# Kernel optimization log

Measured on AMD Instinct MI355X. Metric: run time of the kernel, lower is better.

The kernel has to match this reference:

```python
import jax, jax.numpy as jnp
import numpy as np

N_FFT = 2048
HOP = 512
WIN = 2048
PAD = N_FFT // 2  # center padding, n_fft // 2


def setup_inputs() -> dict:
    key = jax.random.key(0)
    x = jax.random.normal(key, (16, 262144), dtype=jnp.float32)
    # periodic Hann window, identical to torch.hann_window(2048)
    window = (0.5 - 0.5 * jnp.cos(2.0 * jnp.pi * jnp.arange(WIN) / WIN)).astype(jnp.float32)
    return {"x": x, "window": window}


def reference(x, window):
    # x: [B, T]; center reflect-pad by n_fft//2 on both sides (matches F.pad mode='reflect')
    xp = jnp.pad(x, ((0, 0), (PAD, PAD)), mode="reflect")
    n_frames = (xp.shape[-1] - N_FFT) // HOP + 1  # static
    # strided framing (replaces the identity-conv im2col in the original)
    idx = jnp.arange(n_frames)[:, None] * HOP + jnp.arange(N_FFT)[None, :]  # [F, n_fft]
    frames = xp[:, idx] * window  # [B, F, n_fft], windowed frames
    # windowed DFT; rfft of windowed frame == F.linear(frames, fft_k) in the original
    spec = jnp.fft.rfft(frames, axis=-1)  # [B, F, n_fft//2+1] complex
    real = jnp.real(spec).transpose(0, 2, 1)  # [B, dim, F]
    imag = jnp.imag(spec).transpose(0, 2, 1)  # [B, dim, F]
    return (real, imag)
```

## Files before the change

### kernel.cpp

```cpp
#include <hip/hip_runtime.h>


#define N_FFT   2048
#define LOG2N   11
#define HOP     512
#define PADL    1024
#define NBINS   1025
#define NFRAMES 513
#define NBATCH  16
#define TLEN    262144

#define HALF_OUT ((size_t)NBATCH * NBINS * NFRAMES)

__device__ __forceinline__ int pidx(int a) { return a + (a >> 5); }

__device__ __forceinline__ int refl(int j) {
    if (j < 0)          j = -j;
    else if (j >= TLEN) j = 2 * TLEN - 2 - j;
    return j;
}

__device__ __forceinline__ float2 cmul(float2 a, float2 w) {
    return make_float2(fmaf(a.x, w.x, -a.y * w.y), fmaf(a.x, w.y, a.y * w.x));
}
__device__ __forceinline__ float2 cadd(float2 a, float2 b) {
    return make_float2(a.x + b.x, a.y + b.y);
}
__device__ __forceinline__ float2 csub(float2 a, float2 b) {
    return make_float2(a.x - b.x, a.y - b.y);
}
__device__ __forceinline__ float2 csqr(float2 w) {
    return make_float2(fmaf(w.x, w.x, -w.y * w.y), 2.0f * w.x * w.y);
}

template <int H, int L2H>
__device__ __forceinline__ void octet_pass(float2* __restrict__ zc, int q) {
    const int p    = q & (H - 1);
    const int base = ((q >> L2H) << (L2H + 3)) + p;
    int ia[8];
#pragma unroll
    for (int m = 0; m < 8; ++m) ia[m] = pidx(base + m * H);
    float2 v0 = zc[ia[0]], v1 = zc[ia[1]], v2 = zc[ia[2]], v3 = zc[ia[3]];
    float2 v4 = zc[ia[4]], v5 = zc[ia[5]], v6 = zc[ia[6]], v7 = zc[ia[7]];

    float2 w1, w2, w3;
    if (H == 1) {
        w3 = make_float2(1.0f, 0.0f); w2 = w3; w1 = w3;
    } else {
        float s, c;
        __sincosf((float)p * (-3.14159265358979323846f / (4.0f * (float)H)), &s, &c);
        w3 = make_float2(c, s);
        w2 = csqr(w3);
        w1 = csqr(w2);
    }

    float2 t;
    t = cmul(v1, w1); v1 = csub(v0, t); v0 = cadd(v0, t);
    t = cmul(v3, w1); v3 = csub(v2, t); v2 = cadd(v2, t);
    t = cmul(v5, w1); v5 = csub(v4, t); v4 = cadd(v4, t);
    t = cmul(v7, w1); v7 = csub(v6, t); v6 = cadd(v6, t);
    const float2 w2m = make_float2(w2.y, -w2.x);
    t = cmul(v2, w2);  v2 = csub(v0, t); v0 = cadd(v0, t);
    t = cmul(v3, w2m); v3 = csub(v1, t); v1 = cadd(v1, t);
    t = cmul(v6, w2);  v6 = csub(v4, t); v4 = cadd(v4, t);
    t = cmul(v7, w2m); v7 = csub(v5, t); v5 = cadd(v5, t);
    const float R = 0.70710678118654752f;
    const float2 w3o  = make_float2((w3.x + w3.y) * R, (w3.y - w3.x) * R);
    const float2 w3m  = make_float2(w3.y, -w3.x);
    const float2 w3mo = make_float2(w3o.y, -w3o.x);
    t = cmul(v4, w3);   v4 = csub(v0, t); v0 = cadd(v0, t);
    t = cmul(v5, w3o);  v5 = csub(v1, t); v1 = cadd(v1, t);
    t = cmul(v6, w3m);  v6 = csub(v2, t); v2 = cadd(v2, t);
    t = cmul(v7, w3mo); v7 = csub(v3, t); v3 = cadd(v3, t);

    zc[ia[0]] = v0; zc[ia[1]] = v1; zc[ia[2]] = v2; zc[ia[3]] = v3;
    zc[ia[4]] = v4; zc[ia[5]] = v5; zc[ia[6]] = v6; zc[ia[7]] = v7;
}

__global__ __launch_bounds__(512, 8) void stft_one(
    const float* __restrict__ x,
    const float* __restrict__ window,
    float* __restrict__ out)
{
    __shared__ float2 z[2][2113];

    const int d = blockIdx.x;
    int b, g;
    if (d >= 2048) {
        b = d - 2048;
        g = 128;
    } else {
        const int xcd  = d & 7;
        const int slot = d >> 3;
        const int O    = (slot >> 3) * 8 + xcd;
        const int L    = O * 8 + (slot & 7);
        b = L >> 7;
        g = L & 127;
    }
    const int tid = threadIdx.x;
    const int f0  = g * 4;
    const int npl = (g == 128) ? 1 : 2;

    const float* xb = x + (size_t)b * TLEN;
    for (int idx = tid; idx < npl * 2048; idx += 512) {
        const int c  = idx >> 11;
        const int n  = idx & 2047;
        const int fa = f0 + 2 * c;
        const float w  = window[n];
        const float va = xb[refl(fa * HOP - PADL + n)] * w;
        const float vb = xb[refl((fa + 1) * HOP - PADL + n)] * w;
        const int r = (int)(__brev((unsigned)n) >> (32 - LOG2N));
        z[c][pidx(r)] = make_float2(va, vb);
    }
    __syncthreads();

    for (int idx = tid; idx < npl * 256; idx += 512)
        octet_pass<1, 0>(z[idx >> 8], idx & 255);
    __syncthreads();
    for (int idx = tid; idx < npl * 256; idx += 512)
        octet_pass<8, 3>(z[idx >> 8], idx & 255);
    __syncthreads();
    for (int idx = tid; idx < npl * 256; idx += 512)
        octet_pass<64, 6>(z[idx >> 8], idx & 255);
    __syncthreads();

    for (int idx = tid; idx < npl * 512; idx += 512) {
        const int c = idx >> 9;
        const int p = idx & 511;
        float s, cc;
        __sincosf((float)p * (-3.14159265358979323846f / 1024.0f), &s, &cc);
        const float2 w2  = make_float2(cc, s);
        const float2 w1  = csqr(w2);
        const float2 w2m = make_float2(w2.y, -w2.x);
        const int i0 = pidx(p), i1 = pidx(p + 512), i2 = pidx(p + 1024), i3 = pidx(p + 1536);
        float2 v0 = z[c][i0], v1 = z[c][i1], v2 = z[c][i2], v3 = z[c][i3];
        float2 t;
        t = cmul(v1, w1); v1 = csub(v0, t); v0 = cadd(v0, t);
        t = cmul(v3, w1); v3 = csub(v2, t); v2 = cadd(v2, t);
        t = cmul(v2, w2);  v2 = csub(v0, t); v0 = cadd(v0, t);
        t = cmul(v3, w2m); v3 = csub(v1, t); v1 = cadd(v1, t);
        z[c][i0] = v0; z[c][i1] = v1; z[c][i2] = v2; z[c][i3] = v3;
    }
    __syncthreads();

    float* __restrict__ outr = out;
    float* __restrict__ outi = out + HALF_OUT;
    if (g < 128) {
        for (int k = tid; k < NBINS; k += 512) {
            const int km = (N_FFT - k) & (N_FFT - 1);
            const float2 zk0 = z[0][pidx(k)];
            const float2 zr0 = z[0][pidx(km)];
            const float2 zk1 = z[1][pidx(k)];
            const float2 zr1 = z[1][pidx(km)];
            const size_t o = ((size_t)b * NBINS + (size_t)k) * NFRAMES + (size_t)f0;
            outr[o + 0] = 0.5f * (zk0.x + zr0.x);
            outr[o + 1] = 0.5f * (zk0.y + zr0.y);
            outr[o + 2] = 0.5f * (zk1.x + zr1.x);
            outr[o + 3] = 0.5f * (zk1.y + zr1.y);
            outi[o + 0] = 0.5f * (zk0.y - zr0.y);
            outi[o + 1] = 0.5f * (zr0.x - zk0.x);
            outi[o + 2] = 0.5f * (zk1.y - zr1.y);
            outi[o + 3] = 0.5f * (zr1.x - zk1.x);
        }
    } else {
        for (int k = tid; k < NBINS; k += 512) {
            const int km = (N_FFT - k) & (N_FFT - 1);
            const float2 zk = z[0][pidx(k)];
            const float2 zr = z[0][pidx(km)];
            const size_t o = ((size_t)b * NBINS + (size_t)k) * NFRAMES + 512;
            outr[o] = 0.5f * (zk.x + zr.x);
            outi[o] = 0.5f * (zk.y - zr.y);
        }
    }
}

extern "C" void kernel_launch(void* const* d_in, const int* in_sizes, int n_in,
                              void* d_out, int out_size, void* d_ws, size_t ws_size,
                              hipStream_t stream) {
    const float* x      = (const float*)d_in[0];
    const float* window = (const float*)d_in[1];
    float* out          = (float*)d_out;

    dim3 grid(2064);
    stft_one<<<grid, 512, 0, stream>>>(x, window, out);
}
```

Baseline: 108.6 us.

## Make each wavefront own an independent FFT sub-block, replacing barriers with lgkmcnt waits

```diff
diff --git a/kernel.cpp b/kernel.cpp
--- a/kernel.cpp
+++ b/kernel.cpp
@@ -11,6 +11,11 @@
 #define TLEN    262144
 
 #define HALF_OUT ((size_t)NBATCH * NBINS * NFRAMES)
+
+#define WFENCE() do { \
+    asm volatile("s_waitcnt lgkmcnt(0)" ::: "memory"); \
+    __builtin_amdgcn_sched_barrier(0); \
+} while (0)
 
 __device__ __forceinline__ int pidx(int a) { return a + (a >> 5); }
 
@@ -101,45 +106,52 @@
     const int f0  = g * 4;
     const int npl = (g == 128) ? 1 : 2;
 
-    const float* xb = x + (size_t)b * TLEN;
-    for (int idx = tid; idx < npl * 2048; idx += 512) {
-        const int c  = idx >> 11;
-        const int n  = idx & 2047;
+    const int l  = tid & 63;
+    const int c  = tid >> 8;
+    const int cc = (tid >> 6) & 3;
+    const int q  = tid & 255;
+
+    if (c < npl) {
+        const float* xb = x + (size_t)b * TLEN;
+        const int nb = ((cc & 1) << 1) | (cc >> 1);
         const int fa = f0 + 2 * c;
-        const float w  = window[n];
-        const float va = xb[refl(fa * HOP - PADL + n)] * w;
-        const float vb = xb[refl((fa + 1) * HOP - PADL + n)] * w;
-        const int r = (int)(__brev((unsigned)n) >> (32 - LOG2N));
-        z[c][pidx(r)] = make_float2(va, vb);
+        const int a0 = fa * HOP - PADL;
+#pragma unroll
+        for (int jj = 0; jj < 8; ++jj) {
+            const int j = (jj << 6) | l;
+            const int n = (j << 2) | nb;
+            const float w  = window[n];
+            const float va = xb[refl(a0 + n)] * w;
+            const float vb = xb[refl(a0 + HOP + n)] * w;
+            const int r = (cc << 9) | (int)(__brev((unsigned)j) >> 23);
+            z[c][pidx(r)] = make_float2(va, vb);
+        }
+
+        WFENCE();
+        octet_pass<1, 0>(z[c], q);
+        WFENCE();
+        octet_pass<8, 3>(z[c], q);
+        WFENCE();
+        octet_pass<64, 6>(z[c], q);
     }
     __syncthreads();
 
-    for (int idx = tid; idx < npl * 256; idx += 512)
-        octet_pass<1, 0>(z[idx >> 8], idx & 255);
-    __syncthreads();
-    for (int idx = tid; idx < npl * 256; idx += 512)
-        octet_pass<8, 3>(z[idx >> 8], idx & 255);
-    __syncthreads();
-    for (int idx = tid; idx < npl * 256; idx += 512)
-        octet_pass<64, 6>(z[idx >> 8], idx & 255);
-    __syncthreads();
-
     for (int idx = tid; idx < npl * 512; idx += 512) {
-        const int c = idx >> 9;
-        const int p = idx & 511;
-        float s, cc;
-        __sincosf((float)p * (-3.14159265358979323846f / 1024.0f), &s, &cc);
-        const float2 w2  = make_float2(cc, s);
+        const int cq = idx >> 9;
+        const int p  = idx & 511;
+        float s, ccs;
+        __sincosf((float)p * (-3.14159265358979323846f / 1024.0f), &s, &ccs);
+        const float2 w2  = make_float2(ccs, s);
         const float2 w1  = csqr(w2);
         const float2 w2m = make_float2(w2.y, -w2.x);
         const int i0 = pidx(p), i1 = pidx(p + 512), i2 = pidx(p + 1024), i3 = pidx(p + 1536);
-        float2 v0 = z[c][i0], v1 = z[c][i1], v2 = z[c][i2], v3 = z[c][i3];
+        float2 v0 = z[cq][i0], v1 = z[cq][i1], v2 = z[cq][i2], v3 = z[cq][i3];
         float2 t;
         t = cmul(v1, w1); v1 = csub(v0, t); v0 = cadd(v0, t);
         t = cmul(v3, w1); v3 = csub(v2, t); v2 = cadd(v2, t);
         t = cmul(v2, w2);  v2 = csub(v0, t); v0 = cadd(v0, t);
         t = cmul(v3, w2m); v3 = csub(v1, t); v1 = cadd(v1, t);
-        z[c][i0] = v0; z[c][i1] = v1; z[c][i2] = v2; z[c][i3] = v3;
+        z[cq][i0] = v0; z[cq][i1] = v1; z[cq][i2] = v2; z[cq][i3] = v3;
     }
     __syncthreads();
 
```

After: 114.8 us. 5.7% more time.

## Process two batches per block and prefetch second batch during first FFT

Applied to the files above, without the earlier changes.

```diff
diff --git a/kernel.cpp b/kernel.cpp
--- a/kernel.cpp
+++ b/kernel.cpp
@@ -18,6 +18,10 @@
     if (j < 0)          j = -j;
     else if (j >= TLEN) j = 2 * TLEN - 2 - j;
     return j;
+}
+
+__device__ __forceinline__ int brev11(int n) {
+    return (int)(__brev((unsigned)n) >> 21);
 }
 
 __device__ __forceinline__ float2 cmul(float2 a, float2 w) {
@@ -77,76 +81,40 @@
     zc[ia[4]] = v4; zc[ia[5]] = v5; zc[ia[6]] = v6; zc[ia[7]] = v7;
 }
 
-__global__ __launch_bounds__(512, 8) void stft_one(
-    const float* __restrict__ x,
-    const float* __restrict__ window,
-    float* __restrict__ out)
-{
-    __shared__ float2 z[2][2113];
-
-    const int d = blockIdx.x;
-    int b, g;
-    if (d >= 2048) {
-        b = d - 2048;
-        g = 128;
-    } else {
-        const int xcd  = d & 7;
-        const int slot = d >> 3;
-        const int O    = (slot >> 3) * 8 + xcd;
-        const int L    = O * 8 + (slot & 7);
-        b = L >> 7;
-        g = L & 127;
-    }
-    const int tid = threadIdx.x;
-    const int f0  = g * 4;
-    const int npl = (g == 128) ? 1 : 2;
-
-    const float* xb = x + (size_t)b * TLEN;
-    for (int idx = tid; idx < npl * 2048; idx += 512) {
-        const int c  = idx >> 11;
-        const int n  = idx & 2047;
-        const int fa = f0 + 2 * c;
-        const float w  = window[n];
-        const float va = xb[refl(fa * HOP - PADL + n)] * w;
-        const float vb = xb[refl((fa + 1) * HOP - PADL + n)] * w;
-        const int r = (int)(__brev((unsigned)n) >> (32 - LOG2N));
-        z[c][pidx(r)] = make_float2(va, vb);
-    }
-    __syncthreads();
-
-    for (int idx = tid; idx < npl * 256; idx += 512)
-        octet_pass<1, 0>(z[idx >> 8], idx & 255);
-    __syncthreads();
-    for (int idx = tid; idx < npl * 256; idx += 512)
-        octet_pass<8, 3>(z[idx >> 8], idx & 255);
-    __syncthreads();
-    for (int idx = tid; idx < npl * 256; idx += 512)
-        octet_pass<64, 6>(z[idx >> 8], idx & 255);
-    __syncthreads();
-
-    for (int idx = tid; idx < npl * 512; idx += 512) {
-        const int c = idx >> 9;
-        const int p = idx & 511;
-        float s, cc;
-        __sincosf((float)p * (-3.14159265358979323846f / 1024.0f), &s, &cc);
-        const float2 w2  = make_float2(cc, s);
-        const float2 w1  = csqr(w2);
-        const float2 w2m = make_float2(w2.y, -w2.x);
-        const int i0 = pidx(p), i1 = pidx(p + 512), i2 = pidx(p + 1024), i3 = pidx(p + 1536);
-        float2 v0 = z[c][i0], v1 = z[c][i1], v2 = z[c][i2], v3 = z[c][i3];
-        float2 t;
-        t = cmul(v1, w1); v1 = csub(v0, t); v0 = cadd(v0, t);
-        t = cmul(v3, w1); v3 = csub(v2, t); v2 = cadd(v2, t);
-        t = cmul(v2, w2);  v2 = csub(v0, t); v0 = cadd(v0, t);
-        t = cmul(v3, w2m); v3 = csub(v1, t); v1 = cadd(v1, t);
-        z[c][i0] = v0; z[c][i1] = v1; z[c][i2] = v2; z[c][i3] = v3;
-    }
-    __syncthreads();
-
-    float* __restrict__ outr = out;
-    float* __restrict__ outi = out + HALF_OUT;
-    if (g < 128) {
-        for (int k = tid; k < NBINS; k += 512) {
+__device__ __forceinline__ void quad_item(float2* __restrict__ zc, int p) {
+    float s, cc;
+    __sincosf((float)p * (-3.14159265358979323846f / 1024.0f), &s, &cc);
+    const float2 w2  = make_float2(cc, s);
+    const float2 w1  = csqr(w2);
+    const float2 w2m = make_float2(w2.y, -w2.x);
+    const int i0 = pidx(p), i1 = pidx(p + 512), i2 = pidx(p + 1024), i3 = pidx(p + 1536);
+    float2 v0 = zc[i0], v1 = zc[i1], v2 = zc[i2], v3 = zc[i3];
+    float2 t;
+    t = cmul(v1, w1); v1 = csub(v0, t); v0 = cadd(v0, t);
+    t = cmul(v3, w1); v3 = csub(v2, t); v2 = cadd(v2, t);
+    t = cmul(v2, w2);  v2 = csub(v0, t); v0 = cadd(v0, t);
+    t = cmul(v3, w2m); v3 = csub(v1, t); v1 = cadd(v1, t);
+    zc[i0] = v0; zc[i1] = v1; zc[i2] = v2; zc[i3] = v3;
+}
+
+__device__ __forceinline__ void fft_main(float2 (*__restrict__ z)[2113], int tid) {
+    const int c = tid >> 8, q = tid & 255;
+    octet_pass<1, 0>(z[c], q);  __syncthreads();
+    octet_pass<8, 3>(z[c], q);  __syncthreads();
+    octet_pass<64, 6>(z[c], q); __syncthreads();
+    quad_item(z[0], tid & 511);
+    quad_item(z[1], tid & 511);
+    __syncthreads();
+}
+
+__device__ __forceinline__ void epi_main(const float2 (*__restrict__ z)[2113],
+                                         float* __restrict__ outr,
+                                         float* __restrict__ outi,
+                                         int b, int f0, int tid) {
+#pragma unroll
+    for (int it = 0; it < 3; ++it) {
+        const int k = tid + it * 512;
+        if (k < NBINS) {
             const int km = (N_FFT - k) & (N_FFT - 1);
             const float2 zk0 = z[0][pidx(k)];
             const float2 zr0 = z[0][pidx(km)];
@@ -162,16 +130,111 @@
             outi[o + 2] = 0.5f * (zk1.y - zr1.y);
             outi[o + 3] = 0.5f * (zr1.x - zk1.x);
         }
-    } else {
-        for (int k = tid; k < NBINS; k += 512) {
-            const int km = (N_FFT - k) & (N_FFT - 1);
-            const float2 zk = z[0][pidx(k)];
-            const float2 zr = z[0][pidx(km)];
-            const size_t o = ((size_t)b * NBINS + (size_t)k) * NFRAMES + 512;
-            outr[o] = 0.5f * (zk.x + zr.x);
-            outi[o] = 0.5f * (zk.y - zr.y);
+    }
+}
+
+__global__ __launch_bounds__(512, 8) void stft_one(
+    const float* __restrict__ x,
+    const float* __restrict__ window,
+    float* __restrict__ out)
+{
+    __shared__ float2 z[2][2113];
+
+    const int d   = blockIdx.x;
+    const int tid = threadIdx.x;
+    float* __restrict__ outr = out;
+    float* __restrict__ outi = out + HALF_OUT;
+
+    if (d < NBATCH) {
+        const int b = d;
+        const float* xb = x + (size_t)b * TLEN;
+        const int a0 = 512 * HOP - PADL;
+#pragma unroll
+        for (int it = 0; it < 4; ++it) {
+            const int n = tid + it * 512;
+            const float w  = window[n];
+            const float va = xb[refl(a0 + n)] * w;
+            const float vb = xb[refl(a0 + HOP + n)] * w;
+            z[0][pidx(brev11(n))] = make_float2(va, vb);
         }
-    }
+        __syncthreads();
+        if (tid < 256) octet_pass<1, 0>(z[0], tid);
+        __syncthreads();
+        if (tid < 256) octet_pass<8, 3>(z[0], tid);
+        __syncthreads();
+        if (tid < 256) octet_pass<64, 6>(z[0], tid);
+        __syncthreads();
+        quad_item(z[0], tid & 511);
+        __syncthreads();
+#pragma unroll
+        for (int it = 0; it < 3; ++it) {
+            const int k = tid + it * 512;
+            if (k < NBINS) {
+                const int km = (N_FFT - k) & (N_FFT - 1);
+                const float2 zk = z[0][pidx(k)];
+                const float2 zr = z[0][pidx(km)];
+                const size_t o = ((size_t)b * NBINS + (size_t)k) * NFRAMES + 512;
+                outr[o] = 0.5f * (zk.x + zr.x);
+                outi[o] = 0.5f * (zk.y - zr.y);
+            }
+        }
+        return;
+    }
+
+    const int m    = d - NBATCH;
+    const int xcd  = m & 7;
+    const int slot = m >> 3;
+    const int O    = (slot >> 3) * 8 + xcd;
+    const int L0   = O * 8 + (slot & 7);
+    const int bA   = L0 >> 7;
+    const int g    = L0 & 127;
+    const int bB   = bA + 8;
+    const int f0   = g * 4;
+
+    const float* xA = x + (size_t)bA * TLEN;
+    const float* xB = x + (size_t)bB * TLEN;
+
+    float w_p[8], pa[8], pb[8];
+
+#pragma unroll
+    for (int it = 0; it < 8; ++it) {
+        const int idx = tid + it * 512;
+        const int c   = idx >> 11;
+        const int n   = idx & 2047;
+        const int fa  = f0 + 2 * c;
+        const float w = window[n];
+        w_p[it] = w;
+        const float va = xA[refl(fa * HOP - PADL + n)] * w;
+        const float vb = xA[refl((fa + 1) * HOP - PADL + n)] * w;
+        z[c][pidx(brev11(n))] = make_float2(va, vb);
+    }
+    __syncthreads();
+
+#pragma unroll
+    for (int it = 0; it < 8; ++it) {
+        const int idx = tid + it * 512;
+        const int c   = idx >> 11;
+        const int n   = idx & 2047;
+        const int fa  = f0 + 2 * c;
+        pa[it] = xB[refl(fa * HOP - PADL + n)];
+        pb[it] = xB[refl((fa + 1) * HOP - PADL + n)];
+    }
+
+    fft_main(z, tid);
+    epi_main(z, outr, outi, bA, f0, tid);
+    __syncthreads();
+
+#pragma unroll
+    for (int it = 0; it < 8; ++it) {
+        const int idx = tid + it * 512;
+        const int c   = idx >> 11;
+        const int n   = idx & 2047;
+        z[c][pidx(brev11(n))] = make_float2(pa[it] * w_p[it], pb[it] * w_p[it]);
+    }
+    __syncthreads();
+
+    fft_main(z, tid);
+    epi_main(z, outr, outi, bB, f0, tid);
 }
 
 extern "C" void kernel_launch(void* const* d_in, const int* in_sizes, int n_in,
@@ -181,6 +244,6 @@
     const float* window = (const float*)d_in[1];
     float* out          = (float*)d_out;
 
-    dim3 grid(2064);
+    dim3 grid(1040);
     stft_one<<<grid, 512, 0, stream>>>(x, window, out);
 }
```

New measurement: 171.3 us. 57.7% more time.
